# Kernel tuning notes

Hardware: AMD Instinct MI355X
Metric: run time of the kernel (lower is better)

Reference implementation:

```python
import jax, jax.numpy as jnp
import numpy as np

N = 100000   # nodes
E = 400000   # edges
G = 64       # graphs in batch
D_IN = 20
D_H = 1024   # 4 * 256
D_FC = 128


def _w(key, shape, fan_in):
    return jax.random.normal(key, shape, jnp.float32) / np.sqrt(fan_in).astype(np.float32)


def setup_inputs() -> dict:
    key = jax.random.key(0)
    ks = jax.random.split(key, 14)
    x = jax.random.normal(ks[0], (N, D_IN), jnp.float32)
    edge_index = jax.random.randint(ks[1], (2, E), 0, N)
    batch = jnp.sort(jax.random.randint(ks[2], (N,), 0, G))
    return {
        "x": x,
        "edge_index": edge_index,
        "batch": batch,
        # SAGEConv 1: lin_l (neighbors, with bias), lin_r (root, no bias)
        "W1l": _w(ks[3], (D_H, D_IN), D_IN),
        "b1l": _w(ks[4], (D_H,), D_IN),
        "W1r": _w(ks[5], (D_H, D_IN), D_IN),
        # SAGEConv 2
        "W2l": _w(ks[6], (D_H, D_H), D_H),
        "b2l": _w(ks[7], (D_H,), D_H),
        "W2r": _w(ks[8], (D_H, D_H), D_H),
        # MLP head
        "Wf1": _w(ks[9], (D_FC, D_H), D_H),
        "bf1": _w(ks[10], (D_FC,), D_H),
        "Wf2": _w(ks[11], (1, D_FC), D_FC),
        "bf2": _w(ks[12], (1,), D_FC),
    }


def _sage_mean(h, src, dst, inv_deg, Wl, bl, Wr):
    # mean over incoming neighbors (src -> dst), then lin_l(agg) + lin_r(h)
    agg = jax.ops.segment_sum(h[src], dst, num_segments=N) * inv_deg  # [N, d]
    return agg @ Wl.T + bl + h @ Wr.T


def reference(x, edge_index, batch, W1l, b1l, W1r, W2l, b2l, W2r, Wf1, bf1, Wf2, bf2):
    src, dst = edge_index[0], edge_index[1]
    deg = jax.ops.segment_sum(jnp.ones((E,), jnp.float32), dst, num_segments=N)
    inv_deg = (1.0 / jnp.maximum(deg, 1.0))[:, None]  # nodes w/o in-edges -> 0 agg

    h = jnp.tanh(_sage_mean(x, src, dst, inv_deg, W1l, b1l, W1r))
    h = jnp.tanh(_sage_mean(h, src, dst, inv_deg, W2l, b2l, W2r))
    g = jax.ops.segment_sum(h, batch, num_segments=G)            # global_add_pool [G, D_H]
    y = jax.nn.leaky_relu(g @ Wf1.T + bf1, negative_slope=0.2)
    return y @ Wf2.T + bf2                                        # [G, 1]
```

## Files before the change

### kernel.cpp

```cpp
#include <hip/hip_runtime.h>
#include <stdint.h>
#include <stddef.h>

#define N_NODES 100000
#define N_EDGES 400000
#define NG      64
#define DIN     20
#define DH      1024
#define DFC     128
#define M_PAD   100096
#define MTILES  782
#define NBLK    391
#define CHUNK_T 128

typedef __attribute__((ext_vector_type(8))) short bf16x8_t;
typedef __attribute__((ext_vector_type(4))) float f32x4_t;

__device__ __forceinline__ float bf2f(uint32_t u){
  union { uint32_t i; float f; } v; v.i = u << 16; return v.f;
}
__device__ __forceinline__ uint32_t pk_bf16(float lo, float hi){
  uint32_t r;
  asm("v_cvt_pk_bf16_f32 %0, %1, %2" : "=v"(r) : "v"(lo), "v"(hi));
  return r;
}
__device__ __forceinline__ float tanhf_fast(float x){
  float t = __expf(2.0f * x);
  return 1.0f - 2.0f * __builtin_amdgcn_rcpf(1.0f + t);
}
__device__ __forceinline__ void gll16(const void* g, void* l){
  __builtin_amdgcn_global_load_lds(
      (const __attribute__((address_space(1))) unsigned int*)g,
      (__attribute__((address_space(3))) unsigned int*)l, 16, 0, 0);
}
__device__ __forceinline__ int xcd_swz(int bid, int nwg){
  if (nwg & 7) return bid;
  return (bid & 7) * (nwg >> 3) + (bid >> 3);
}
#define BARRIER() asm volatile("s_barrier" ::: "memory")

__global__ void k_diag(float* __restrict__ out, float v){
  out[threadIdx.x] = v;
}

__global__ void k_deg(const int* __restrict__ dstn, int* __restrict__ deg){
  int e = blockIdx.x * 256 + threadIdx.x;
  if (e < N_EDGES) atomicAdd(&deg[dstn[e]], 1);
}

__global__ void k_scan1(const int* __restrict__ deg, int* __restrict__ rowoff,
                        int* __restrict__ part){
  __shared__ int sb[256];
  const int t = threadIdx.x;
  const int n = blockIdx.x * 256 + t;
  int v = (n < N_NODES) ? deg[n] : 0;
  sb[t] = v;
  __syncthreads();
  for (int off = 1; off < 256; off <<= 1){
    int u = (t >= off) ? sb[t - off] : 0;
    __syncthreads();
    sb[t] += u;
    __syncthreads();
  }
  int incl = sb[t];
  if (n < N_NODES) rowoff[n] = incl - v;
  if (t == 255) part[blockIdx.x] = incl;
}

__global__ void k_scan2(int* part, int nblk){
  __shared__ int sb[512];
  const int t = threadIdx.x;
  int v = (t < nblk) ? part[t] : 0;
  sb[t] = v;
  __syncthreads();
  for (int off = 1; off < 512; off <<= 1){
    int u = (t >= off) ? sb[t - off] : 0;
    __syncthreads();
    sb[t] += u;
    __syncthreads();
  }
  if (t < nblk) part[t] = sb[t] - v;
}

__global__ void k_scan3(int* __restrict__ rowoff, const int* __restrict__ part){
  int n = blockIdx.x * 256 + threadIdx.x;
  if (n < N_NODES) rowoff[n] += part[blockIdx.x];
  if (n == 0) rowoff[N_NODES] = N_EDGES;
}

__global__ void k_fill(const int* __restrict__ src, const int* __restrict__ dstn,
                       const int* __restrict__ rowoff, int* __restrict__ cursor,
                       int* __restrict__ colx){
  int e = blockIdx.x * 256 + threadIdx.x;
  if (e < N_EDGES){
    int d = dstn[e];
    int p = rowoff[d] + atomicAdd(&cursor[d], 1);
    colx[p] = src[e];
  }
}

__global__ void k_pack(const float* __restrict__ x, const int* __restrict__ rowoff,
                       const int* __restrict__ colx, uint16_t* __restrict__ Ap){
  const int n = blockIdx.x * 256 + threadIdx.x;
  if (n >= M_PAD) return;
  uint4 o[8];
  if (n < N_NODES){
    f32x4_t a0 = {}, a1 = {}, a2 = {}, a3 = {}, a4 = {};
    const int e0 = rowoff[n], e1 = rowoff[n + 1];
    for (int e = e0; e < e1; e++){
      const f32x4_t* xr = (const f32x4_t*)(x + (size_t)colx[e] * DIN);
      a0 += xr[0]; a1 += xr[1]; a2 += xr[2]; a3 += xr[3]; a4 += xr[4];
    }
    const float inv = (e1 > e0) ? 1.f / (float)(e1 - e0) : 0.f;
    a0 *= inv; a1 *= inv; a2 *= inv; a3 *= inv; a4 *= inv;
    const f32x4_t* xs = (const f32x4_t*)(x + (size_t)n * DIN);
    f32x4_t b0 = xs[0], b1 = xs[1], b2 = xs[2], b3 = xs[3], b4 = xs[4];
    o[0] = make_uint4(pk_bf16(a0[0],a0[1]), pk_bf16(a0[2],a0[3]), pk_bf16(a1[0],a1[1]), pk_bf16(a1[2],a1[3]));
    o[1] = make_uint4(pk_bf16(a2[0],a2[1]), pk_bf16(a2[2],a2[3]), pk_bf16(a3[0],a3[1]), pk_bf16(a3[2],a3[3]));
    o[2] = make_uint4(pk_bf16(a4[0],a4[1]), pk_bf16(a4[2],a4[3]), pk_bf16(b0[0],b0[1]), pk_bf16(b0[2],b0[3]));
    o[3] = make_uint4(pk_bf16(b1[0],b1[1]), pk_bf16(b1[2],b1[3]), pk_bf16(b2[0],b2[1]), pk_bf16(b2[2],b2[3]));
    o[4] = make_uint4(pk_bf16(b3[0],b3[1]), pk_bf16(b3[2],b3[3]), pk_bf16(b4[0],b4[1]), pk_bf16(b4[2],b4[3]));
    o[5] = make_uint4(0,0,0,0); o[6] = o[5]; o[7] = o[5];
  } else {
    o[0] = make_uint4(0,0,0,0);
    for (int i = 1; i < 8; i++) o[i] = o[0];
  }
  uint4* dst = (uint4*)(Ap + (size_t)n * 64);
#pragma unroll
  for (int i = 0; i < 8; i++) dst[i] = o[i];
}

__global__ void k_prep(const float* __restrict__ W1l, const float* __restrict__ W1r,
                       uint16_t* __restrict__ Bp,
                       const float* __restrict__ W2l, const float* __restrict__ W2r,
                       uint16_t* __restrict__ B2){
  const int b = blockIdx.x;
  if (b < 4){
    const int j = b * 256 + threadIdx.x;
    if (j >= DH) return;
    const f32x4_t* wl = (const f32x4_t*)(W1l + (size_t)j * DIN);
    const f32x4_t* wr = (const f32x4_t*)(W1r + (size_t)j * DIN);
    f32x4_t a0 = wl[0], a1 = wl[1], a2 = wl[2], a3 = wl[3], a4 = wl[4];
    f32x4_t b0 = wr[0], b1 = wr[1], b2 = wr[2], b3 = wr[3], b4 = wr[4];
    uint4 o[8];
    o[0] = make_uint4(pk_bf16(a0[0],a0[1]), pk_bf16(a0[2],a0[3]), pk_bf16(a1[0],a1[1]), pk_bf16(a1[2],a1[3]));
    o[1] = make_uint4(pk_bf16(a2[0],a2[1]), pk_bf16(a2[2],a2[3]), pk_bf16(a3[0],a3[1]), pk_bf16(a3[2],a3[3]));
    o[2] = make_uint4(pk_bf16(a4[0],a4[1]), pk_bf16(a4[2],a4[3]), pk_bf16(b0[0],b0[1]), pk_bf16(b0[2],b0[3]));
    o[3] = make_uint4(pk_bf16(b1[0],b1[1]), pk_bf16(b1[2],b1[3]), pk_bf16(b2[0],b2[1]), pk_bf16(b2[2],b2[3]));
    o[4] = make_uint4(pk_bf16(b3[0],b3[1]), pk_bf16(b3[2],b3[3]), pk_bf16(b4[0],b4[1]), pk_bf16(b4[2],b4[3]));
    o[5] = make_uint4(0,0,0,0); o[6] = o[5]; o[7] = o[5];
    uint4* dst = (uint4*)(Bp + (size_t)j * 64);
#pragma unroll
    for (int i = 0; i < 8; i++) dst[i] = o[i];
    return;
  }
  int q = (b - 4) * 256 + threadIdx.x;
  const int sel = q >= 262144;
  if (sel) q -= 262144;
  const int j = q >> 8;
  const int k4 = (q & 255) * 4;
  const float* w = sel ? W2r : W2l;
  float4 f = *(const float4*)(w + (size_t)j * 1024 + k4);
  uint2 o;
  o.x = pk_bf16(f.x, f.y);
  o.y = pk_bf16(f.z, f.w);
  *(uint2*)(B2 + (size_t)j * 2048 + sel * 1024 + k4) = o;
}

__global__ __launch_bounds__(256) void k_l1g(
    const uint16_t* __restrict__ Ap, const uint16_t* __restrict__ Bp,
    const float* __restrict__ bias, uint16_t* __restrict__ h1)
{
  __shared__ uint16_t lds[16384];
  const int wg = xcd_swz(blockIdx.x, gridDim.x);
  const int mt = wg >> 3, jt = wg & 7;
  const int tid = threadIdx.x;
  const int lane = tid & 63, w = tid >> 6;
  const int wm = w >> 1, wn = w & 1;
  char* ldsb = (char*)lds;

  const int rgrp = lane >> 3;
  const int sl   = lane & 7;
  const int sw   = sl ^ rgrp;
#pragma unroll
  for (int t = 0; t < 4; t++){
    const int r0 = w * 32 + t * 8;
    gll16((const char*)Ap + (size_t)(mt * 128 + r0 + rgrp) * 128 + sw * 16,
          ldsb + r0 * 128);
    gll16((const char*)Bp + (size_t)(jt * 128 + r0 + rgrp) * 128 + sw * 16,
          ldsb + 16384 + r0 * 128);
  }
  __syncthreads();

  f32x4_t acc[4][4] = {};
  const int ks = lane >> 4;
  const int rA = wm * 64 + (lane & 15);
  const int rB = wn * 64 + (lane & 15);
#pragma unroll
  for (int kt = 0; kt < 2; kt++){
    bf16x8_t af[4], bg[4];
#pragma unroll
    for (int mi = 0; mi < 4; mi++){
      int r = rA + mi * 16;
      af[mi] = *(const bf16x8_t*)(ldsb + r * 128 + (((kt * 4 + ks) ^ (r & 7)) << 4));
    }
#pragma unroll
    for (int ni = 0; ni < 4; ni++){
      int r = rB + ni * 16;
      bg[ni] = *(const bf16x8_t*)(ldsb + 16384 + r * 128 + (((kt * 4 + ks) ^ (r & 7)) << 4));
    }
#pragma unroll
    for (int mi = 0; mi < 4; mi++)
#pragma unroll
      for (int ni = 0; ni < 4; ni++)
        acc[mi][ni] = __builtin_amdgcn_mfma_f32_16x16x32_bf16(bg[ni], af[mi], acc[mi][ni], 0, 0, 0);
  }

  __syncthreads();
  const int c4 = (lane >> 4) * 4;
#pragma unroll
  for (int ni = 0; ni < 4; ni++){
    const int colL = wn * 64 + ni * 16 + c4;
    const f32x4_t bs = *(const f32x4_t*)(bias + jt * 128 + colL);
    const int b16 = colL >> 3;
    const int hh  = (colL >> 2) & 1;
#pragma unroll
    for (int mi = 0; mi < 4; mi++){
      const int r = wm * 64 + mi * 16 + (lane & 15);
      uint2 o;
      o.x = pk_bf16(tanhf_fast(acc[mi][ni][0] + bs[0]), tanhf_fast(acc[mi][ni][1] + bs[1]));
      o.y = pk_bf16(tanhf_fast(acc[mi][ni][2] + bs[2]), tanhf_fast(acc[mi][ni][3] + bs[3]));
      *(uint2*)(ldsb + r * 256 + ((b16 ^ (r & 15)) << 4) + hh * 8) = o;
    }
  }
  __syncthreads();
  char* dst0 = (char*)(h1 + (size_t)(mt * 128) * DH + jt * 128);
#pragma unroll
  for (int k = 0; k < 8; k++){
    const int c = tid + k * 256;
    const int r = c >> 4, b16 = c & 15;
    uint4 v = *(const uint4*)(ldsb + r * 256 + ((b16 ^ (r & 15)) << 4));
    *(uint4*)(dst0 + (size_t)r * DH * 2 + b16 * 16) = v;
  }
}

__global__ void k_agg2(const uint16_t* __restrict__ h1, const int* __restrict__ rowoff,
                       const int* __restrict__ colx, uint16_t* __restrict__ aggc,
                       int row0){
  const int half = threadIdx.x >> 7;
  const int t = threadIdx.x & 127;
  const int nl = blockIdx.x * 2 + half;
  const int n = row0 + nl;
  uint4* out = (uint4*)aggc;
  const size_t ro = (size_t)nl * 128 + t;
  if (n >= N_NODES){ out[ro] = make_uint4(0u,0u,0u,0u); return; }
  const int e0 = rowoff[n], e1 = rowoff[n + 1];
  float f0=0.f,f1=0.f,f2=0.f,f3=0.f,f4=0.f,f5=0.f,f6=0.f,f7=0.f;
  const uint4* H = (const uint4*)h1;
  for (int e = e0; e < e1; e++){
    uint4 u = H[(size_t)colx[e] * 128 + t];
    f0 += bf2f(u.x); f1 += bf2f(u.x >> 16);
    f2 += bf2f(u.y); f3 += bf2f(u.y >> 16);
    f4 += bf2f(u.z); f5 += bf2f(u.z >> 16);
    f6 += bf2f(u.w); f7 += bf2f(u.w >> 16);
  }
  const float inv = (e1 > e0) ? 1.f / (float)(e1 - e0) : 0.f;
  uint4 o;
  o.x = pk_bf16(f0 * inv, f1 * inv);
  o.y = pk_bf16(f2 * inv, f3 * inv);
  o.z = pk_bf16(f4 * inv, f5 * inv);
  o.w = pk_bf16(f6 * inv, f7 * inv);
  out[ro] = o;
}

__global__ __launch_bounds__(512) void k_gemm(
    const uint16_t* __restrict__ A0, const uint16_t* __restrict__ A1,
    const uint16_t* __restrict__ B2, const float* __restrict__ bias,
    const int* __restrict__ batch, float* __restrict__ gbuf, int row0)
{
  __shared__ char ldsb[131072];
  const int wg = xcd_swz(blockIdx.x, gridDim.x);
  const int mt = wg >> 2, jtg = wg & 3;
  const int tid = threadIdx.x;
  const int lane = tid & 63, w = tid >> 6;
  const int wm = w >> 2, wn = w & 3;

  const int aw_row = w * 8 + (lane >> 3);
  const size_t slotb = (size_t)(((lane & 7) ^ (lane >> 3)) << 4);

  auto stageA = [&](int half, int t2){
    const char* gb = (t2 < 16) ? (const char*)A0 : (const char*)A1;
    const size_t ktc = (size_t)(t2 & 15) * 128;
    char* lb = ldsb + (t2 & 1) * 65536 + half * 16384 + w * 1024;
    const size_t r0 = (size_t)(mt * 256 + half * 128 + aw_row);
    gll16(gb + r0 * 2048 + ktc + slotb, lb);
    gll16(gb + (r0 + 64) * 2048 + ktc + slotb, lb + 8192);
  };
  auto stageB = [&](int half, int t2){
    const size_t ktc = (size_t)t2 * 128;
    char* lb = ldsb + (t2 & 1) * 65536 + 32768 + half * 16384 + w * 1024;
    const size_t r0 = (size_t)(jtg * 256 + half * 128 + aw_row);
    gll16((const char*)B2 + r0 * 4096 + ktc + slotb, lb);
    gll16((const char*)B2 + (r0 + 64) * 4096 + ktc + slotb, lb + 8192);
  };

  stageB(0, 0); stageB(1, 0); stageA(0, 0); stageA(1, 0);
  stageB(0, 1); stageB(1, 1); stageA(0, 1);
  asm volatile("s_waitcnt vmcnt(6)" ::: "memory");
  BARRIER();

  f32x4_t acc[8][4] = {};
  const int ks = lane >> 4;
  const int rA = wm * 128 + (lane & 15);
  const int rB = wn * 64 + (lane & 15);

  for (int kt = 0; kt < 32; ++kt){
    const char* lA = ldsb + (kt & 1) * 65536;
    const char* lB = lA + 32768;
    bf16x8_t bg[4][2], af03a[4], af03b[4], af47a[4], af47b[4];
#pragma unroll
    for (int n = 0; n < 4; n++){
      int r = rB + n * 16;
      bg[n][0] = *(const bf16x8_t*)(lB + r * 128 + ((ks ^ (r & 7)) << 4));
      bg[n][1] = *(const bf16x8_t*)(lB + r * 128 + (((4 + ks) ^ (r & 7)) << 4));
    }
#pragma unroll
    for (int m = 0; m < 4; m++){
      int r = rA + m * 16;
      af03a[m] = *(const bf16x8_t*)(lA + r * 128 + ((ks ^ (r & 7)) << 4));
    }
    if (kt < 31) stageA(1, kt + 1);
    BARRIER();
    __builtin_amdgcn_s_setprio(1);
#pragma unroll
    for (int m = 0; m < 4; m++)
#pragma unroll
      for (int n = 0; n < 4; n++)
        acc[m][n] = __builtin_amdgcn_mfma_f32_16x16x32_bf16(af03a[m], bg[n][0], acc[m][n], 0, 0, 0);
    __builtin_amdgcn_s_setprio(0);
    BARRIER();
#pragma unroll
    for (int m = 0; m < 4; m++){
      int r = rA + m * 16;
      af03b[m] = *(const bf16x8_t*)(lA + r * 128 + (((4 + ks) ^ (r & 7)) << 4));
    }
#pragma unroll
    for (int m = 0; m < 4; m++){
      int r = rA + 64 + m * 16;
      af47a[m] = *(const bf16x8_t*)(lA + r * 128 + ((ks ^ (r & 7)) << 4));
    }
    if (kt < 30) stageB(0, kt + 2);
    BARRIER();
    __builtin_amdgcn_s_setprio(1);
#pragma unroll
    for (int m = 0; m < 4; m++)
#pragma unroll
      for (int n = 0; n < 4; n++)
        acc[4 + m][n] = __builtin_amdgcn_mfma_f32_16x16x32_bf16(af47a[m], bg[n][0], acc[4 + m][n], 0, 0, 0);
    __builtin_amdgcn_s_setprio(0);
    BARRIER();
#pragma unroll
    for (int m = 0; m < 4; m++){
      int r = rA + 64 + m * 16;
      af47b[m] = *(const bf16x8_t*)(lA + r * 128 + (((4 + ks) ^ (r & 7)) << 4));
    }
    if (kt < 30) stageB(1, kt + 2);
    BARRIER();
    __builtin_amdgcn_s_setprio(1);
#pragma unroll
    for (int m = 0; m < 4; m++)
#pragma unroll
      for (int n = 0; n < 4; n++)
        acc[m][n] = __builtin_amdgcn_mfma_f32_16x16x32_bf16(af03b[m], bg[n][1], acc[m][n], 0, 0, 0);
    __builtin_amdgcn_s_setprio(0);
    BARRIER();
    if (kt < 30){
      stageA(0, kt + 2);
      asm volatile("s_waitcnt vmcnt(6)" ::: "memory");
    } else {
      asm volatile("s_waitcnt vmcnt(0)" ::: "memory");
    }
    BARRIER();
    __builtin_amdgcn_s_setprio(1);
#pragma unroll
    for (int m = 0; m < 4; m++)
#pragma unroll
      for (int n = 0; n < 4; n++)
        acc[4 + m][n] = __builtin_amdgcn_mfma_f32_16x16x32_bf16(af47b[m], bg[n][1], acc[4 + m][n], 0, 0, 0);
    __builtin_amdgcn_s_setprio(0);
    BARRIER();
  }

  const int rowbase = row0 + mt * 256 + wm * 128;
  const int colbase = jtg * 256 + wn * 64;
  int bt[8][4];
#pragma unroll
  for (int mi = 0; mi < 8; mi++)
#pragma unroll
    for (int i = 0; i < 4; i++){
      int R = rowbase + mi * 16 + (lane >> 4) * 4 + i;
      bt[mi][i] = (R < N_NODES) ? batch[R] : -1;
    }
  const int c0 = rowbase       < N_NODES ? rowbase       : N_NODES - 1;
  const int c1 = rowbase + 127 < N_NODES ? rowbase + 127 : N_NODES - 1;
  const int gmin = batch[c0], gmax = batch[c1];

#pragma unroll
  for (int ni = 0; ni < 4; ni++){
    const int col = colbase + ni * 16 + (lane & 15);
    const float bs = bias[col];
    float v[8][4];
#pragma unroll
    for (int mi = 0; mi < 8; mi++)
#pragma unroll
      for (int i = 0; i < 4; i++)
        v[mi][i] = tanhf_fast(acc[mi][ni][i] + bs);
    for (int g = gmin; g <= gmax; g++){
      float s_ = 0.f;
#pragma unroll
      for (int mi = 0; mi < 8; mi++)
#pragma unroll
        for (int i = 0; i < 4; i++)
          s_ += (bt[mi][i] == g) ? v[mi][i] : 0.f;
      s_ += __shfl_xor(s_, 16);
      s_ += __shfl_xor(s_, 32);
      if (lane < 16) atomicAdd(&gbuf[g * DH + col], s_);
    }
  }
}

__global__ void k_head(const float* __restrict__ gbuf, const float* __restrict__ Wf1,
                       const float* __restrict__ bf1, const float* __restrict__ Wf2,
                       const float* __restrict__ bf2, float* __restrict__ out){
  const int gg = blockIdx.x, j = threadIdx.x;
  const float* grow = gbuf + (size_t)gg * DH;
  const float* wr = Wf1 + (size_t)j * DH;
  float acc = bf1[j];
  for (int k = 0; k < DH; k++) acc = fmaf(grow[k], wr[k], acc);
  float y = acc > 0.f ? acc : 0.2f * acc;
  __shared__ float sb[DFC];
  sb[j] = y * Wf2[j];
  __syncthreads();
  for (int off = 64; off > 0; off >>= 1){
    if (j < off) sb[j] += sb[j + off];
    __syncthreads();
  }
  if (j == 0) out[gg] = sb[0] + bf2[0];
}

extern "C" void kernel_launch(void* const* d_in, const int* in_sizes, int n_in,
                              void* d_out, int out_size, void* d_ws, size_t ws_size,
                              hipStream_t stream){
  const float* x   = (const float*)d_in[0];
  const int*   ei  = (const int*)d_in[1];
  const int*   src = ei;
  const int*   dst = ei + N_EDGES;
  const int*   batch = (const int*)d_in[2];
  const float* W1l = (const float*)d_in[3];
  const float* b1l = (const float*)d_in[4];
  const float* W1r = (const float*)d_in[5];
  const float* W2l = (const float*)d_in[6];
  const float* b2l = (const float*)d_in[7];
  const float* W2r = (const float*)d_in[8];
  const float* Wf1 = (const float*)d_in[9];
  const float* bf1 = (const float*)d_in[10];
  const float* Wf2 = (const float*)d_in[11];
  const float* bf2 = (const float*)d_in[12];
  float* out = (float*)d_out;
  (void)in_sizes; (void)n_in; (void)out_size;

  char* ws = (char*)d_ws;
  size_t off = 0;
  auto alloc = [&](size_t bytes) -> void* {
    void* p = (void*)(ws + off);
    off = (off + bytes + 255) & ~(size_t)255;
    return p;
  };
  uint16_t* h1   = (uint16_t*)alloc((size_t)M_PAD * DH * 2);
  uint16_t* Ap   = (uint16_t*)alloc((size_t)M_PAD * 64 * 2);
  uint16_t* Bp   = (uint16_t*)alloc((size_t)DH * 64 * 2);
  uint16_t* B2   = (uint16_t*)alloc((size_t)DH * 2048 * 2);
  int*      deg  = (int*)alloc((size_t)N_NODES * 4);
  int*      curs = (int*)alloc((size_t)N_NODES * 4);
  float*    gbuf = (float*)alloc((size_t)NG * DH * 4);
  int*      rowo = (int*)alloc((size_t)(N_NODES + 1) * 4);
  int*      colx = (int*)alloc((size_t)N_EDGES * 4);
  int*      part = (int*)alloc((size_t)NBLK * 4);
  long long remain = (long long)ws_size - (long long)off;
  int chunk_t = (int)(remain / (128LL * 2048LL));
  if (chunk_t > CHUNK_T) chunk_t = CHUNK_T;
  chunk_t &= ~1;
  if (chunk_t < 2){
    k_diag<<<1, 64, 0, stream>>>(out, (float)ws_size);
    return;
  }
  uint16_t* aggc = (uint16_t*)alloc((size_t)chunk_t * 128 * DH * 2);

  const size_t zset = (size_t)((char*)gbuf - (char*)deg) + (size_t)NG * DH * 4;
  hipMemsetAsync(deg, 0, zset, stream);

  k_deg  <<<(N_EDGES + 255) / 256, 256, 0, stream>>>(dst, deg);
  k_scan1<<<NBLK, 256, 0, stream>>>(deg, rowo, part);
  k_scan2<<<1, 512, 0, stream>>>(part, NBLK);
  k_scan3<<<NBLK, 256, 0, stream>>>(rowo, part);
  k_fill <<<(N_EDGES + 255) / 256, 256, 0, stream>>>(src, dst, rowo, curs, colx);
  k_pack <<<NBLK, 256, 0, stream>>>(x, rowo, colx, Ap);
  k_prep <<<4 + 2048, 256, 0, stream>>>(W1l, W1r, Bp, W2l, W2r, B2);
  k_l1g  <<<MTILES * 8, 256, 0, stream>>>(Ap, Bp, b1l, h1);

  for (int t0 = 0; t0 < MTILES; ){
    int ct = MTILES - t0 < chunk_t ? MTILES - t0 : chunk_t;
    int row0 = t0 * 128;
    k_agg2<<<ct * 64, 256, 0, stream>>>(h1, rowo, colx, aggc, row0);
    k_gemm<<<(ct / 2) * 4, 512, 0, stream>>>(aggc, h1 + (size_t)row0 * DH,
                                             B2, b2l, batch, gbuf, row0);
    t0 += ct;
  }
  k_head <<<NG, DFC, 0, stream>>>(gbuf, Wf1, bf1, Wf2, bf2, out);
}
```

Before: 756.1 us.

## Collapse GEMM k-step into one LDS read phase and one MFMA phase

Restructures the main bf16 MFMA loop of the 1024x1024 GEMM. All A fragments for both k-halves are now loaded up front, and all global-to-LDS staging for the next stages is issued together. The 64 MFMAs then run back-to-back, which cuts the per-k-step barrier count from eight to two. This removes synchronisation overhead and scheduling bubbles between small MFMA groups, but it gives up the finer interleaving of LDS reads with MFMA. It also raises register pressure from holding more fragments live, and it risks an LDS hazard because staging into the current buffer is issued before the last fragment reads.

```diff
diff --git a/kernel.cpp b/kernel.cpp
--- a/kernel.cpp
+++ b/kernel.cpp
@@ -317,7 +317,7 @@
   for (int kt = 0; kt < 32; ++kt){
     const char* lA = ldsb + (kt & 1) * 65536;
     const char* lB = lA + 32768;
-    bf16x8_t bg[4][2], af03a[4], af03b[4], af47a[4], af47b[4];
+    bf16x8_t bg[4][2], af03[4][2], af47[4][2];
 #pragma unroll
     for (int n = 0; n < 4; n++){
       int r = rB + n * 16;
@@ -327,67 +327,44 @@
 #pragma unroll
     for (int m = 0; m < 4; m++){
       int r = rA + m * 16;
-      af03a[m] = *(const bf16x8_t*)(lA + r * 128 + ((ks ^ (r & 7)) << 4));
-    }
+      af03[m][0] = *(const bf16x8_t*)(lA + r * 128 + ((ks ^ (r & 7)) << 4));
+      af03[m][1] = *(const bf16x8_t*)(lA + r * 128 + (((4 + ks) ^ (r & 7)) << 4));
+    }
+    asm volatile("s_waitcnt lgkmcnt(0)" ::: "memory");
+    __builtin_amdgcn_sched_barrier(0);
+    BARRIER();
     if (kt < 31) stageA(1, kt + 1);
-    BARRIER();
-    __builtin_amdgcn_s_setprio(1);
-#pragma unroll
-    for (int m = 0; m < 4; m++)
-#pragma unroll
-      for (int n = 0; n < 4; n++)
-        acc[m][n] = __builtin_amdgcn_mfma_f32_16x16x32_bf16(af03a[m], bg[n][0], acc[m][n], 0, 0, 0);
-    __builtin_amdgcn_s_setprio(0);
-    BARRIER();
-#pragma unroll
-    for (int m = 0; m < 4; m++){
-      int r = rA + m * 16;
-      af03b[m] = *(const bf16x8_t*)(lA + r * 128 + (((4 + ks) ^ (r & 7)) << 4));
-    }
+    if (kt < 30){ stageB(0, kt + 2); stageB(1, kt + 2); stageA(0, kt + 2); }
 #pragma unroll
     for (int m = 0; m < 4; m++){
       int r = rA + 64 + m * 16;
-      af47a[m] = *(const bf16x8_t*)(lA + r * 128 + ((ks ^ (r & 7)) << 4));
-    }
-    if (kt < 30) stageB(0, kt + 2);
-    BARRIER();
+      af47[m][0] = *(const bf16x8_t*)(lA + r * 128 + ((ks ^ (r & 7)) << 4));
+      af47[m][1] = *(const bf16x8_t*)(lA + r * 128 + (((4 + ks) ^ (r & 7)) << 4));
+    }
     __builtin_amdgcn_s_setprio(1);
 #pragma unroll
     for (int m = 0; m < 4; m++)
 #pragma unroll
       for (int n = 0; n < 4; n++)
-        acc[4 + m][n] = __builtin_amdgcn_mfma_f32_16x16x32_bf16(af47a[m], bg[n][0], acc[4 + m][n], 0, 0, 0);
+        acc[m][n] = __builtin_amdgcn_mfma_f32_16x16x32_bf16(af03[m][0], bg[n][0], acc[m][n], 0, 0, 0);
+#pragma unroll
+    for (int m = 0; m < 4; m++)
+#pragma unroll
+      for (int n = 0; n < 4; n++)
+        acc[m][n] = __builtin_amdgcn_mfma_f32_16x16x32_bf16(af03[m][1], bg[n][1], acc[m][n], 0, 0, 0);
+#pragma unroll
+    for (int m = 0; m < 4; m++)
+#pragma unroll
+      for (int n = 0; n < 4; n++)
+        acc[4 + m][n] = __builtin_amdgcn_mfma_f32_16x16x32_bf16(af47[m][0], bg[n][0], acc[4 + m][n], 0, 0, 0);
+#pragma unroll
+    for (int m = 0; m < 4; m++)
+#pragma unroll
+      for (int n = 0; n < 4; n++)
+        acc[4 + m][n] = __builtin_amdgcn_mfma_f32_16x16x32_bf16(af47[m][1], bg[n][1], acc[4 + m][n], 0, 0, 0);
     __builtin_amdgcn_s_setprio(0);
-    BARRIER();
-#pragma unroll
-    for (int m = 0; m < 4; m++){
-      int r = rA + 64 + m * 16;
-      af47b[m] = *(const bf16x8_t*)(lA + r * 128 + (((4 + ks) ^ (r & 7)) << 4));
-    }
-    if (kt < 30) stageB(1, kt + 2);
-    BARRIER();
-    __builtin_amdgcn_s_setprio(1);
-#pragma unroll
-    for (int m = 0; m < 4; m++)
-#pragma unroll
-      for (int n = 0; n < 4; n++)
-        acc[m][n] = __builtin_amdgcn_mfma_f32_16x16x32_bf16(af03b[m], bg[n][1], acc[m][n], 0, 0, 0);
-    __builtin_amdgcn_s_setprio(0);
-    BARRIER();
-    if (kt < 30){
-      stageA(0, kt + 2);
-      asm volatile("s_waitcnt vmcnt(6)" ::: "memory");
-    } else {
-      asm volatile("s_waitcnt vmcnt(0)" ::: "memory");
-    }
-    BARRIER();
-    __builtin_amdgcn_s_setprio(1);
-#pragma unroll
-    for (int m = 0; m < 4; m++)
-#pragma unroll
-      for (int n = 0; n < 4; n++)
-        acc[4 + m][n] = __builtin_amdgcn_mfma_f32_16x16x32_bf16(af47b[m], bg[n][1], acc[4 + m][n], 0, 0, 0);
-    __builtin_amdgcn_s_setprio(0);
+    if (kt < 30) asm volatile("s_waitcnt vmcnt(6)" ::: "memory");
+    else         asm volatile("s_waitcnt vmcnt(0)" ::: "memory");
     BARRIER();
   }
 
```

Measured after the change: 775.0 us. +2.5%, slower.
